# Optimization experiments

Hardware: AMD Instinct MI355X
Metric: run time of the kernel (lower is better)

Reference implementation:

```python
import jax, jax.numpy as jnp
import numpy as np

N = 50000
E = 800000
IN_DIM = 128
HID = 32
HEADS = 4
OUT_DIM = 32
NEG_SLOPE = 0.2


def setup_inputs() -> dict:
    key = jax.random.key(0)
    ks = jax.random.split(key, 10)
    x = jax.random.normal(ks[0], (N, IN_DIM), dtype=jnp.float32)
    edge_index = jax.random.randint(ks[1], (2, E), 0, N, dtype=jnp.int64)
    # layer 1: in 128 -> 4 heads x 32, concat
    W1 = jax.random.normal(ks[2], (IN_DIM, HEADS * HID), dtype=jnp.float32) * (1.0 / np.sqrt(IN_DIM))
    a_src1 = jax.random.normal(ks[3], (HEADS, HID), dtype=jnp.float32) * 0.1
    a_dst1 = jax.random.normal(ks[4], (HEADS, HID), dtype=jnp.float32) * 0.1
    b1 = jnp.zeros((HEADS * HID,), dtype=jnp.float32)
    # layer 2: in 128 -> 1 head x 32, mean
    W2 = jax.random.normal(ks[5], (HEADS * HID, OUT_DIM), dtype=jnp.float32) * (1.0 / np.sqrt(HEADS * HID))
    a_src2 = jax.random.normal(ks[6], (1, OUT_DIM), dtype=jnp.float32) * 0.1
    a_dst2 = jax.random.normal(ks[7], (1, OUT_DIM), dtype=jnp.float32) * 0.1
    b2 = jnp.zeros((OUT_DIM,), dtype=jnp.float32)
    return {"x": x, "edge_index": edge_index, "W1": W1, "a_src1": a_src1,
            "a_dst1": a_dst1, "b1": b1, "W2": W2, "a_src2": a_src2,
            "a_dst2": a_dst2, "b2": b2}


def gat_layer(x, src, dst, W, a_src, a_dst, b, heads, concat, num_nodes):
    # linear transform -> [N, H, C]
    h = (x @ W).reshape(num_nodes, heads, -1)
    # per-node attention halves, gathered per edge -> [E, H]
    alpha = jax.nn.leaky_relu((h * a_src).sum(-1)[src] + (h * a_dst).sum(-1)[dst],
                              negative_slope=NEG_SLOPE)
    # segment softmax over edges grouped by destination node
    seg_max = jax.ops.segment_max(alpha, dst, num_segments=num_nodes)
    e = jnp.exp(alpha - seg_max[dst])
    denom = jax.ops.segment_sum(e, dst, num_segments=num_nodes)[dst]
    w = e / jnp.maximum(denom, 1e-16)
    # weighted message scatter-sum -> [N, H, C]
    out = jax.ops.segment_sum(h[src] * w[..., None], dst, num_segments=num_nodes)
    out = out.reshape(num_nodes, -1) if concat else out.mean(axis=1)
    return out + b


def reference(x, edge_index, W1, a_src1, a_dst1, b1, W2, a_src2, a_dst2, b2):
    num_nodes = x.shape[0]
    loops = jnp.arange(num_nodes, dtype=edge_index.dtype)
    src = jnp.concatenate([edge_index[0], loops])  # add self-loops (PyG default)
    dst = jnp.concatenate([edge_index[1], loops])
    h = jax.nn.relu(gat_layer(x, src, dst, W1, a_src1, a_dst1, b1, HEADS, True, num_nodes))
    out = gat_layer(h, src, dst, W2, a_src2, a_dst2, b2, 1, False, num_nodes)
    return jax.nn.sigmoid(out)
```

## Files before the change

### kernel.cpp

```cpp
#include <hip/hip_runtime.h>
#include <math.h>

#define NN 50000
#define NE 800000
#define NT (NN + NE)
#define SCAN_BLOCKS 196

__device__ __forceinline__ float lrelu(float a) { return a > 0.f ? a : 0.2f * a; }

__device__ __forceinline__ int edge_val(const void* eb, int is64, long long i) {
  return is64 ? (int)((const unsigned int*)eb)[i << 1] : ((const int*)eb)[i];
}

__device__ __forceinline__ float sel4(float4 v, int h) {
  float r = v.x;
  r = (h == 1) ? v.y : r;
  r = (h == 2) ? v.z : r;
  r = (h == 3) ? v.w : r;
  return r;
}

__device__ __forceinline__ unsigned int f2bf(float f) {
  unsigned int u = __float_as_uint(f);
  return (u + 0x7FFFu + ((u >> 16) & 1u)) >> 16;
}
__device__ __forceinline__ unsigned int packbf(float lo, float hi) {
  return f2bf(lo) | (f2bf(hi) << 16);
}
__device__ __forceinline__ float bflo(unsigned int v) { return __uint_as_float(v << 16); }
__device__ __forceinline__ float bfhi(unsigned int v) { return __uint_as_float(v & 0xFFFF0000u); }

__global__ void k_detect(const unsigned int* __restrict__ eb, int* __restrict__ flag) {
  __shared__ int nz;
  if (threadIdx.x == 0) nz = 0;
  __syncthreads();
  int local = 0;
  for (int i = threadIdx.x; i < 2048; i += 256) local |= (eb[2 * i + 1] != 0u);
  if (local) nz = 1;
  __syncthreads();
  if (threadIdx.x == 0) *flag = (nz == 0) ? 1 : 0;
}

__global__ void k_hist(const void* __restrict__ eb, const int* __restrict__ flag,
                       int* __restrict__ cnt) {
  int e = blockIdx.x * 256 + threadIdx.x;
  if (e >= NT) return;
  int is64 = *flag;
  int d = (e < NE) ? edge_val(eb, is64, (long long)NE + e) : (e - NE);
  atomicAdd(&cnt[d], 1);
}

__global__ __launch_bounds__(256) void k_bsum(const int* __restrict__ cnt,
                                              int* __restrict__ bsum) {
  int i = blockIdx.x * 256 + threadIdx.x;
  int v = (i < NN) ? cnt[i] : 0;
#pragma unroll
  for (int off = 1; off < 64; off <<= 1) v += __shfl_xor(v, off, 64);
  __shared__ int ws[4];
  int lane = threadIdx.x & 63, wid = threadIdx.x >> 6;
  if (lane == 0) ws[wid] = v;
  __syncthreads();
  if (threadIdx.x == 0) bsum[blockIdx.x] = ws[0] + ws[1] + ws[2] + ws[3];
}

__global__ __launch_bounds__(256) void k_bscan(const int* __restrict__ bsum,
                                               int* __restrict__ boff,
                                               int* __restrict__ rowp) {
  int t = threadIdx.x;
  int lane = t & 63, wid = t >> 6;
  int v = (t < SCAN_BLOCKS) ? bsum[t] : 0;
  int incl = v;
#pragma unroll
  for (int off = 1; off < 64; off <<= 1) {
    int u = __shfl_up(incl, off, 64);
    if (lane >= off) incl += u;
  }
  __shared__ int wsum[4], woff[4];
  if (lane == 63) wsum[wid] = incl;
  __syncthreads();
  if (t == 0) {
    woff[0] = 0;
    woff[1] = wsum[0];
    woff[2] = wsum[0] + wsum[1];
    woff[3] = wsum[0] + wsum[1] + wsum[2];
  }
  __syncthreads();
  if (t < SCAN_BLOCKS) boff[t] = woff[wid] + incl - v;
  if (t == 0) rowp[NN] = NT;
}

__global__ __launch_bounds__(256) void k_rowp(const int* __restrict__ cnt,
                                              const int* __restrict__ boff,
                                              int* __restrict__ rowp,
                                              int* __restrict__ nxt) {
  int i = blockIdx.x * 256 + threadIdx.x;
  int t = threadIdx.x;
  int lane = t & 63, wid = t >> 6;
  int v = (i < NN) ? cnt[i] : 0;
  int incl = v;
#pragma unroll
  for (int off = 1; off < 64; off <<= 1) {
    int u = __shfl_up(incl, off, 64);
    if (lane >= off) incl += u;
  }
  __shared__ int wsum[4], woff[4];
  if (lane == 63) wsum[wid] = incl;
  __syncthreads();
  if (t == 0) {
    woff[0] = 0;
    woff[1] = wsum[0];
    woff[2] = wsum[0] + wsum[1];
    woff[3] = wsum[0] + wsum[1] + wsum[2];
  }
  __syncthreads();
  if (i < NN) {
    int e = boff[blockIdx.x] + woff[wid] + incl - v;
    rowp[i] = e;
    nxt[i] = e;
  }
}

__global__ void k_scatter(const void* __restrict__ eb, const int* __restrict__ flag,
                          int* __restrict__ nxt, int* __restrict__ csr) {
  int e = blockIdx.x * 256 + threadIdx.x;
  if (e >= NT) return;
  int is64 = *flag;
  int s, d;
  if (e < NE) {
    s = edge_val(eb, is64, e);
    d = edge_val(eb, is64, (long long)NE + e);
  } else {
    s = d = e - NE;
  }
  int pos = atomicAdd(&nxt[d], 1);
  csr[pos] = s;
}

__global__ __launch_bounds__(256) void k_gemm1(const float* __restrict__ X,
                                               const float* __restrict__ W,
                                               const float* __restrict__ a_src,
                                               const float* __restrict__ a_dst,
                                               uint4* __restrict__ Hb,
                                               float* __restrict__ AS,
                                               float* __restrict__ AD) {
  __shared__ float xs[64][36];
  __shared__ float ws[32][132];
  int tid = threadIdx.x;
  int tx = tid & 15, ty = tid >> 4;
  int r0 = blockIdx.x * 64;
  float acc[4][8];
#pragma unroll
  for (int i = 0; i < 4; ++i)
#pragma unroll
    for (int j = 0; j < 8; ++j) acc[i][j] = 0.f;

  for (int kb = 0; kb < 4; ++kb) {
    __syncthreads();
#pragma unroll
    for (int i = tid; i < 512; i += 256) {
      int row = i >> 3, c4 = i & 7;
      int gr = r0 + row;
      float4 v = make_float4(0.f, 0.f, 0.f, 0.f);
      if (gr < NN) v = ((const float4*)X)[(size_t)gr * 32 + kb * 8 + c4];
      *(float4*)&xs[row][c4 * 4] = v;
    }
#pragma unroll
    for (int i = tid; i < 1024; i += 256) {
      int kr = i >> 5, c4 = i & 31;
      *(float4*)&ws[kr][c4 * 4] = ((const float4*)W)[(size_t)(kb * 32 + kr) * 32 + c4];
    }
    __syncthreads();
#pragma unroll 4
    for (int k = 0; k < 32; ++k) {
      float xr[4];
#pragma unroll
      for (int i = 0; i < 4; ++i) xr[i] = xs[ty * 4 + i][k];
      float4 w0 = *(const float4*)&ws[k][tx * 8];
      float4 w1 = *(const float4*)&ws[k][tx * 8 + 4];
#pragma unroll
      for (int i = 0; i < 4; ++i) {
        acc[i][0] += xr[i] * w0.x;
        acc[i][1] += xr[i] * w0.y;
        acc[i][2] += xr[i] * w0.z;
        acc[i][3] += xr[i] * w0.w;
        acc[i][4] += xr[i] * w1.x;
        acc[i][5] += xr[i] * w1.y;
        acc[i][6] += xr[i] * w1.z;
        acc[i][7] += xr[i] * w1.w;
      }
    }
  }
  float4 s0 = ((const float4*)a_src)[tx * 2];
  float4 s1 = ((const float4*)a_src)[tx * 2 + 1];
  float4 d0 = ((const float4*)a_dst)[tx * 2];
  float4 d1 = ((const float4*)a_dst)[tx * 2 + 1];
  int head = tx >> 2;
#pragma unroll
  for (int i = 0; i < 4; ++i) {
    int gr = r0 + ty * 4 + i;
    float ps = acc[i][0] * s0.x + acc[i][1] * s0.y + acc[i][2] * s0.z + acc[i][3] * s0.w +
               acc[i][4] * s1.x + acc[i][5] * s1.y + acc[i][6] * s1.z + acc[i][7] * s1.w;
    float pd = acc[i][0] * d0.x + acc[i][1] * d0.y + acc[i][2] * d0.z + acc[i][3] * d0.w +
               acc[i][4] * d1.x + acc[i][5] * d1.y + acc[i][6] * d1.z + acc[i][7] * d1.w;
    ps += __shfl_xor(ps, 1, 64);
    ps += __shfl_xor(ps, 2, 64);
    pd += __shfl_xor(pd, 1, 64);
    pd += __shfl_xor(pd, 2, 64);
    if (gr < NN) {
      Hb[(size_t)gr * 16 + tx] =
          make_uint4(packbf(acc[i][0], acc[i][1]), packbf(acc[i][2], acc[i][3]),
                     packbf(acc[i][4], acc[i][5]), packbf(acc[i][6], acc[i][7]));
      if ((tx & 3) == 0) {
        AS[gr * 4 + head] = ps;
        AD[gr * 4 + head] = pd;
      }
    }
  }
}

__global__ __launch_bounds__(256) void k_l1node(const int* __restrict__ rowp,
                                                const int* __restrict__ csr,
                                                const uint4* __restrict__ Hb,
                                                const float* __restrict__ AS,
                                                const float* __restrict__ AD,
                                                const float* __restrict__ b1,
                                                float* __restrict__ HM) {
  int lane = threadIdx.x & 63, wid = threadIdx.x >> 6;
  int n = blockIdx.x * 4 + wid;
  if (n >= NN) return;
  int beg = rowp[n], end = rowp[n + 1];
  float4 ad4 = *(const float4*)&AD[n * 4];

  int sl = lane & 15;
  int g = lane >> 4;
  int hd = sl >> 2;
  float adh = sel4(ad4, hd);

  float a0 = 0.f, a1 = 0.f, a2 = 0.f, a3 = 0.f, a4 = 0.f, a5 = 0.f, a6 = 0.f, a7 = 0.f;
  float esum = 0.f;
  int i = beg + g;
  for (; i + 4 < end; i += 8) {
    int sA = csr[i];
    int sB = csr[i + 4];
    float lA = AS[sA * 4 + hd];
    float lB = AS[sB * 4 + hd];
    uint4 hA = Hb[(size_t)sA * 16 + sl];
    uint4 hB = Hb[(size_t)sB * 16 + sl];
    float wA = __expf(lrelu(lA + adh));
    float wB = __expf(lrelu(lB + adh));
    esum += wA + wB;
    a0 += wA * bflo(hA.x) + wB * bflo(hB.x);
    a1 += wA * bfhi(hA.x) + wB * bfhi(hB.x);
    a2 += wA * bflo(hA.y) + wB * bflo(hB.y);
    a3 += wA * bfhi(hA.y) + wB * bfhi(hB.y);
    a4 += wA * bflo(hA.z) + wB * bflo(hB.z);
    a5 += wA * bfhi(hA.z) + wB * bfhi(hB.z);
    a6 += wA * bflo(hA.w) + wB * bflo(hB.w);
    a7 += wA * bfhi(hA.w) + wB * bfhi(hB.w);
  }
  if (i < end) {
    int s = csr[i];
    float l = AS[s * 4 + hd];
    uint4 hv = Hb[(size_t)s * 16 + sl];
    float w0 = __expf(lrelu(l + adh));
    esum += w0;
    a0 += w0 * bflo(hv.x);
    a1 += w0 * bfhi(hv.x);
    a2 += w0 * bflo(hv.y);
    a3 += w0 * bfhi(hv.y);
    a4 += w0 * bflo(hv.z);
    a5 += w0 * bfhi(hv.z);
    a6 += w0 * bflo(hv.w);
    a7 += w0 * bfhi(hv.w);
  }
#pragma unroll
  for (int off = 16; off < 64; off <<= 1) {
    esum += __shfl_xor(esum, off, 64);
    a0 += __shfl_xor(a0, off, 64);
    a1 += __shfl_xor(a1, off, 64);
    a2 += __shfl_xor(a2, off, 64);
    a3 += __shfl_xor(a3, off, 64);
    a4 += __shfl_xor(a4, off, 64);
    a5 += __shfl_xor(a5, off, 64);
    a6 += __shfl_xor(a6, off, 64);
    a7 += __shfl_xor(a7, off, 64);
  }
  if (lane < 16) {
    float r = 1.f / esum;
    int c = sl * 8;
    float4 bva = *(const float4*)&b1[c];
    float4 bvb = *(const float4*)&b1[c + 4];
    *(float4*)&HM[(size_t)n * 128 + c] =
        make_float4(fmaxf(a0 * r + bva.x, 0.f), fmaxf(a1 * r + bva.y, 0.f),
                    fmaxf(a2 * r + bva.z, 0.f), fmaxf(a3 * r + bva.w, 0.f));
    *(float4*)&HM[(size_t)n * 128 + c + 4] =
        make_float4(fmaxf(a4 * r + bvb.x, 0.f), fmaxf(a5 * r + bvb.y, 0.f),
                    fmaxf(a6 * r + bvb.z, 0.f), fmaxf(a7 * r + bvb.w, 0.f));
  }
}

__global__ __launch_bounds__(256) void k_gemm2(const float* __restrict__ HM,
                                               const float* __restrict__ W2,
                                               const float* __restrict__ a_src2,
                                               const float* __restrict__ a_dst2,
                                               uint4* __restrict__ Hb2,
                                               float* __restrict__ AS,
                                               float* __restrict__ AD) {
  __shared__ float wsm[128 * 32];
  __shared__ float xs[256][33];
  int tid = threadIdx.x;
  for (int i = tid; i < 1024; i += 256) ((float4*)wsm)[i] = ((const float4*)W2)[i];
  int r = blockIdx.x * 256 + tid;
  float acc[32];
#pragma unroll
  for (int j = 0; j < 32; ++j) acc[j] = 0.f;

  for (int kb = 0; kb < 4; ++kb) {
    __syncthreads();
#pragma unroll
    for (int i = tid; i < 2048; i += 256) {
      int row = i >> 3, c4 = i & 7;
      int gr = blockIdx.x * 256 + row;
      float4 v = make_float4(0.f, 0.f, 0.f, 0.f);
      if (gr < NN) v = ((const float4*)HM)[(size_t)gr * 32 + kb * 8 + c4];
      float* p = &xs[row][c4 * 4];
      p[0] = v.x; p[1] = v.y; p[2] = v.z; p[3] = v.w;
    }
    __syncthreads();
#pragma unroll 4
    for (int k = 0; k < 32; ++k) {
      float xv = xs[tid][k];
      const float4* wr = (const float4*)&wsm[(kb * 32 + k) * 32];
#pragma unroll
      for (int j4 = 0; j4 < 8; ++j4) {
        float4 wv = wr[j4];
        acc[j4 * 4 + 0] += xv * wv.x;
        acc[j4 * 4 + 1] += xv * wv.y;
        acc[j4 * 4 + 2] += xv * wv.z;
        acc[j4 * 4 + 3] += xv * wv.w;
      }
    }
  }
  if (r < NN) {
    float ps = 0.f, pd = 0.f;
    unsigned int pk[16];
#pragma unroll
    for (int j4 = 0; j4 < 8; ++j4) {
      float4 sv = ((const float4*)a_src2)[j4];
      float4 dv = ((const float4*)a_dst2)[j4];
      ps += acc[j4 * 4 + 0] * sv.x + acc[j4 * 4 + 1] * sv.y +
            acc[j4 * 4 + 2] * sv.z + acc[j4 * 4 + 3] * sv.w;
      pd += acc[j4 * 4 + 0] * dv.x + acc[j4 * 4 + 1] * dv.y +
            acc[j4 * 4 + 2] * dv.z + acc[j4 * 4 + 3] * dv.w;
      pk[j4 * 2]     = packbf(acc[j4 * 4 + 0], acc[j4 * 4 + 1]);
      pk[j4 * 2 + 1] = packbf(acc[j4 * 4 + 2], acc[j4 * 4 + 3]);
    }
#pragma unroll
    for (int q = 0; q < 4; ++q)
      Hb2[(size_t)r * 4 + q] =
          make_uint4(pk[q * 4], pk[q * 4 + 1], pk[q * 4 + 2], pk[q * 4 + 3]);
    AS[r] = ps;
    AD[r] = pd;
  }
}

__global__ __launch_bounds__(256) void k_l2node(const int* __restrict__ rowp,
                                                const int* __restrict__ csr,
                                                const uint2* __restrict__ Hb2,
                                                const float* __restrict__ AS,
                                                const float* __restrict__ AD,
                                                const float* __restrict__ b2,
                                                float* __restrict__ out) {
  int lane = threadIdx.x & 63, wid = threadIdx.x >> 6;
  int n = blockIdx.x * 4 + wid;
  if (n >= NN) return;
  int beg = rowp[n], end = rowp[n + 1];
  float adn = AD[n];

  int sl = lane & 7;
  int g = lane >> 3;
  float a0 = 0.f, a1 = 0.f, a2 = 0.f, a3 = 0.f;
  float esum = 0.f;
  int i = beg + g;
  for (; i + 8 < end; i += 16) {
    int sA = csr[i];
    int sB = csr[i + 8];
    float lA = AS[sA];
    float lB = AS[sB];
    uint2 hA = Hb2[(size_t)sA * 8 + sl];
    uint2 hB = Hb2[(size_t)sB * 8 + sl];
    float wA = __expf(lrelu(lA + adn));
    float wB = __expf(lrelu(lB + adn));
    esum += wA + wB;
    a0 += wA * bflo(hA.x) + wB * bflo(hB.x);
    a1 += wA * bfhi(hA.x) + wB * bfhi(hB.x);
    a2 += wA * bflo(hA.y) + wB * bflo(hB.y);
    a3 += wA * bfhi(hA.y) + wB * bfhi(hB.y);
  }
  if (i < end) {
    int s = csr[i];
    float l = AS[s];
    uint2 hv = Hb2[(size_t)s * 8 + sl];
    float w0 = __expf(lrelu(l + adn));
    esum += w0;
    a0 += w0 * bflo(hv.x);
    a1 += w0 * bfhi(hv.x);
    a2 += w0 * bflo(hv.y);
    a3 += w0 * bfhi(hv.y);
  }
#pragma unroll
  for (int off = 8; off < 64; off <<= 1) {
    esum += __shfl_xor(esum, off, 64);
    a0 += __shfl_xor(a0, off, 64);
    a1 += __shfl_xor(a1, off, 64);
    a2 += __shfl_xor(a2, off, 64);
    a3 += __shfl_xor(a3, off, 64);
  }
  if (lane < 8) {
    float r = 1.f / esum;
    int c = sl * 4;
    float4 bv = *(const float4*)&b2[c];
    float vx = a0 * r + bv.x, vy = a1 * r + bv.y, vz = a2 * r + bv.z, vw = a3 * r + bv.w;
    *(float4*)&out[(size_t)n * 32 + c] =
        make_float4(1.f / (1.f + __expf(-vx)), 1.f / (1.f + __expf(-vy)),
                    1.f / (1.f + __expf(-vz)), 1.f / (1.f + __expf(-vw)));
  }
}

extern "C" void kernel_launch(void* const* d_in, const int* in_sizes, int n_in,
                              void* d_out, int out_size, void* d_ws, size_t ws_size,
                              hipStream_t stream) {
  (void)in_sizes; (void)n_in; (void)out_size; (void)ws_size;
  const float* x      = (const float*)d_in[0];
  const void*  eb     = d_in[1];
  const float* W1     = (const float*)d_in[2];
  const float* a_src1 = (const float*)d_in[3];
  const float* a_dst1 = (const float*)d_in[4];
  const float* b1     = (const float*)d_in[5];
  const float* W2     = (const float*)d_in[6];
  const float* a_src2 = (const float*)d_in[7];
  const float* a_dst2 = (const float*)d_in[8];
  const float* b2     = (const float*)d_in[9];
  float* out = (float*)d_out;

  char* w = (char*)d_ws;
  auto alloc = [&](size_t bytes) {
    char* p = w;
    w += (bytes + 255) & ~(size_t)255;
    return p;
  };
  int*   flag = (int*)alloc(4);
  int*   cnt  = (int*)alloc((size_t)NN * 4);
  int*   rowp = (int*)alloc((size_t)(NN + 1) * 4);
  int*   nxt  = (int*)alloc((size_t)NN * 4);
  int*   csr  = (int*)alloc((size_t)NT * 4);
  int*   bsum = (int*)alloc((size_t)SCAN_BLOCKS * 4);
  int*   boff = (int*)alloc((size_t)SCAN_BLOCKS * 4);
  uint4* Hb1  = (uint4*)alloc((size_t)NN * 128 * 2);
  float* AS1  = (float*)alloc((size_t)NN * 16);
  float* AD1  = (float*)alloc((size_t)NN * 16);
  float* HM   = (float*)alloc((size_t)NN * 128 * 4);
  uint4* Hb2 = Hb1;
  float* AS2 = (float*)cnt;
  float* AD2 = (float*)nxt;

  hipMemsetAsync(cnt, 0, (size_t)NN * 4, stream);
  k_detect<<<1, 256, 0, stream>>>((const unsigned int*)eb, flag);
  int egrid = (NT + 255) / 256;
  k_hist<<<egrid, 256, 0, stream>>>(eb, flag, cnt);
  k_bsum<<<SCAN_BLOCKS, 256, 0, stream>>>(cnt, bsum);
  k_bscan<<<1, 256, 0, stream>>>(bsum, boff, rowp);
  k_rowp<<<SCAN_BLOCKS, 256, 0, stream>>>(cnt, boff, rowp, nxt);
  k_scatter<<<egrid, 256, 0, stream>>>(eb, flag, nxt, csr);

  k_gemm1<<<(NN + 63) / 64, 256, 0, stream>>>(x, W1, a_src1, a_dst1, Hb1, AS1, AD1);
  k_l1node<<<(NN + 3) / 4, 256, 0, stream>>>(rowp, csr, Hb1, AS1, AD1, b1, HM);
  k_gemm2<<<(NN + 255) / 256, 256, 0, stream>>>(HM, W2, a_src2, a_dst2, Hb2, AS2, AD2);
  k_l2node<<<(NN + 3) / 4, 256, 0, stream>>>(rowp, csr, (const uint2*)Hb2, AS2, AD2, b2, out);
}
```

Baseline: 326.8 us.

## Record histogram slot positions to drop the atomic scatter pass in CSR build

```diff
diff --git a/kernel.cpp b/kernel.cpp
--- a/kernel.cpp
+++ b/kernel.cpp
@@ -7,10 +7,6 @@
 #define SCAN_BLOCKS 196
 
 __device__ __forceinline__ float lrelu(float a) { return a > 0.f ? a : 0.2f * a; }
-
-__device__ __forceinline__ int edge_val(const void* eb, int is64, long long i) {
-  return is64 ? (int)((const unsigned int*)eb)[i << 1] : ((const int*)eb)[i];
-}
 
 __device__ __forceinline__ float sel4(float4 v, int h) {
   float r = v.x;
@@ -41,13 +37,31 @@
   if (threadIdx.x == 0) *flag = (nz == 0) ? 1 : 0;
 }
 
-__global__ void k_hist(const void* __restrict__ eb, const int* __restrict__ flag,
-                       int* __restrict__ cnt) {
-  int e = blockIdx.x * 256 + threadIdx.x;
-  if (e >= NT) return;
+__global__ __launch_bounds__(256) void k_pass1(const void* __restrict__ eb,
+                                               const int* __restrict__ flag,
+                                               int* __restrict__ cnt,
+                                               unsigned int* __restrict__ pw) {
+  int e0 = (blockIdx.x * 256 + threadIdx.x) * 4;
+  if (e0 >= NT) return;
   int is64 = *flag;
-  int d = (e < NE) ? edge_val(eb, is64, (long long)NE + e) : (e - NE);
-  atomicAdd(&cnt[d], 1);
+  int d0, d1, d2, d3;
+  if (e0 < NE) {
+    if (is64) {
+      const uint4* p = (const uint4*)((const unsigned int*)eb + 2 * ((size_t)NE + e0));
+      uint4 a = p[0], b = p[1];
+      d0 = (int)a.x; d1 = (int)a.z; d2 = (int)b.x; d3 = (int)b.z;
+    } else {
+      int4 v = *(const int4*)((const int*)eb + (size_t)NE + e0);
+      d0 = v.x; d1 = v.y; d2 = v.z; d3 = v.w;
+    }
+  } else {
+    d0 = e0 - NE; d1 = d0 + 1; d2 = d0 + 2; d3 = d0 + 3;
+  }
+  unsigned int p0 = (unsigned int)atomicAdd(&cnt[d0], 1);
+  unsigned int p1 = (unsigned int)atomicAdd(&cnt[d1], 1);
+  unsigned int p2 = (unsigned int)atomicAdd(&cnt[d2], 1);
+  unsigned int p3 = (unsigned int)atomicAdd(&cnt[d3], 1);
+  *(uint4*)&pw[e0] = make_uint4(p0, p1, p2, p3);
 }
 
 __global__ __launch_bounds__(256) void k_bsum(const int* __restrict__ cnt,
@@ -91,8 +105,7 @@
 
 __global__ __launch_bounds__(256) void k_rowp(const int* __restrict__ cnt,
                                               const int* __restrict__ boff,
-                                              int* __restrict__ rowp,
-                                              int* __restrict__ nxt) {
+                                              int* __restrict__ rowp) {
   int i = blockIdx.x * 256 + threadIdx.x;
   int t = threadIdx.x;
   int lane = t & 63, wid = t >> 6;
@@ -113,27 +126,43 @@
     woff[3] = wsum[0] + wsum[1] + wsum[2];
   }
   __syncthreads();
-  if (i < NN) {
-    int e = boff[blockIdx.x] + woff[wid] + incl - v;
-    rowp[i] = e;
-    nxt[i] = e;
-  }
-}
-
-__global__ void k_scatter(const void* __restrict__ eb, const int* __restrict__ flag,
-                          int* __restrict__ nxt, int* __restrict__ csr) {
-  int e = blockIdx.x * 256 + threadIdx.x;
-  if (e >= NT) return;
+  if (i < NN) rowp[i] = boff[blockIdx.x] + woff[wid] + incl - v;
+}
+
+__global__ __launch_bounds__(256) void k_pass2(const void* __restrict__ eb,
+                                               const int* __restrict__ flag,
+                                               const int* __restrict__ rowp,
+                                               const unsigned int* __restrict__ pw,
+                                               int* __restrict__ csr) {
+  int e0 = (blockIdx.x * 256 + threadIdx.x) * 4;
+  if (e0 >= NT) return;
   int is64 = *flag;
-  int s, d;
-  if (e < NE) {
-    s = edge_val(eb, is64, e);
-    d = edge_val(eb, is64, (long long)NE + e);
+  int s0, s1, s2, s3, d0, d1, d2, d3;
+  if (e0 < NE) {
+    if (is64) {
+      const uint4* ps = (const uint4*)((const unsigned int*)eb + 2 * (size_t)e0);
+      uint4 a = ps[0], b = ps[1];
+      s0 = (int)a.x; s1 = (int)a.z; s2 = (int)b.x; s3 = (int)b.z;
+      const uint4* pd = (const uint4*)((const unsigned int*)eb + 2 * ((size_t)NE + e0));
+      uint4 c = pd[0], d = pd[1];
+      d0 = (int)c.x; d1 = (int)c.z; d2 = (int)d.x; d3 = (int)d.z;
+    } else {
+      int4 vs = *(const int4*)((const int*)eb + (size_t)e0);
+      s0 = vs.x; s1 = vs.y; s2 = vs.z; s3 = vs.w;
+      int4 vd = *(const int4*)((const int*)eb + (size_t)NE + e0);
+      d0 = vd.x; d1 = vd.y; d2 = vd.z; d3 = vd.w;
+    }
   } else {
-    s = d = e - NE;
-  }
-  int pos = atomicAdd(&nxt[d], 1);
-  csr[pos] = s;
+    s0 = d0 = e0 - NE;
+    s1 = d1 = d0 + 1;
+    s2 = d2 = d0 + 2;
+    s3 = d3 = d0 + 3;
+  }
+  uint4 pv = *(const uint4*)&pw[e0];
+  csr[rowp[d0] + (int)pv.x] = s0;
+  csr[rowp[d1] + (int)pv.y] = s1;
+  csr[rowp[d2] + (int)pv.z] = s2;
+  csr[rowp[d3] + (int)pv.w] = s3;
 }
 
 __global__ __launch_bounds__(256) void k_gemm1(const float* __restrict__ X,
@@ -449,29 +478,29 @@
     w += (bytes + 255) & ~(size_t)255;
     return p;
   };
-  int*   flag = (int*)alloc(4);
-  int*   cnt  = (int*)alloc((size_t)NN * 4);
-  int*   rowp = (int*)alloc((size_t)(NN + 1) * 4);
-  int*   nxt  = (int*)alloc((size_t)NN * 4);
-  int*   csr  = (int*)alloc((size_t)NT * 4);
-  int*   bsum = (int*)alloc((size_t)SCAN_BLOCKS * 4);
-  int*   boff = (int*)alloc((size_t)SCAN_BLOCKS * 4);
-  uint4* Hb1  = (uint4*)alloc((size_t)NN * 128 * 2);
-  float* AS1  = (float*)alloc((size_t)NN * 16);
-  float* AD1  = (float*)alloc((size_t)NN * 16);
-  float* HM   = (float*)alloc((size_t)NN * 128 * 4);
+  int*          flag = (int*)alloc(4);
+  int*          cnt  = (int*)alloc((size_t)NN * 4);
+  int*          rowp = (int*)alloc((size_t)(NN + 1) * 4);
+  unsigned int* pw   = (unsigned int*)alloc((size_t)NT * 4);
+  int*          csr  = (int*)alloc((size_t)NT * 4);
+  int*          bsum = (int*)alloc((size_t)SCAN_BLOCKS * 4);
+  int*          boff = (int*)alloc((size_t)SCAN_BLOCKS * 4);
+  uint4*        Hb1  = (uint4*)alloc((size_t)NN * 128 * 2);
+  float*        AS1  = (float*)alloc((size_t)NN * 16);
+  float*        AD1  = (float*)alloc((size_t)NN * 16);
+  float*        HM   = (float*)alloc((size_t)NN * 128 * 4);
   uint4* Hb2 = Hb1;
   float* AS2 = (float*)cnt;
-  float* AD2 = (float*)nxt;
+  float* AD2 = (float*)pw;
 
   hipMemsetAsync(cnt, 0, (size_t)NN * 4, stream);
   k_detect<<<1, 256, 0, stream>>>((const unsigned int*)eb, flag);
-  int egrid = (NT + 255) / 256;
-  k_hist<<<egrid, 256, 0, stream>>>(eb, flag, cnt);
+  int egrid4 = (NT / 4 + 255) / 256;
+  k_pass1<<<egrid4, 256, 0, stream>>>(eb, flag, cnt, pw);
   k_bsum<<<SCAN_BLOCKS, 256, 0, stream>>>(cnt, bsum);
   k_bscan<<<1, 256, 0, stream>>>(bsum, boff, rowp);
-  k_rowp<<<SCAN_BLOCKS, 256, 0, stream>>>(cnt, boff, rowp, nxt);
-  k_scatter<<<egrid, 256, 0, stream>>>(eb, flag, nxt, csr);
+  k_rowp<<<SCAN_BLOCKS, 256, 0, stream>>>(cnt, boff, rowp);
+  k_pass2<<<egrid4, 256, 0, stream>>>(eb, flag, rowp, pw, csr);
 
   k_gemm1<<<(NN + 63) / 64, 256, 0, stream>>>(x, W1, a_src1, a_dst1, Hb1, AS1, AD1);
   k_l1node<<<(NN + 3) / 4, 256, 0, stream>>>(rowp, csr, Hb1, AS1, AD1, b1, HM);
```

New measurement: 282.3 us. 13.6% less time.
